# Optimization experiments

Measured on AMD Instinct MI355X. Metric: run time of the kernel, lower is better.

## Reference

```python
import jax, jax.numpy as jnp
import numpy as np
from jax import lax

KS = 3
N = KS * KS  # 9 sampling points per output pixel
EPS = 1e-5
DN = ('NCHW', 'OIHW', 'NCHW')


def _deform_conv(x, w_off, b_off, w_conv):
    """Pure-PyTorch-style DeformConv2d (padding=0, stride=1, no modulation)."""
    b, c, H, W = x.shape
    dt = x.dtype
    # offset conv: 3x3, padding=1 -> (b, 2N, h, w) with h=H, w=W
    offset = lax.conv_general_dilated(x, w_off, (1, 1), ((1, 1), (1, 1)), dimension_numbers=DN)
    offset = offset + b_off[None, :, None, None]
    h, w = offset.shape[2], offset.shape[3]
    # p_n: kernel-relative offsets in {-1,0,1}^2
    r = jnp.arange(-(KS - 1) // 2, (KS - 1) // 2 + 1, dtype=dt)
    pnx, pny = jnp.meshgrid(r, r, indexing='ij')
    p_n = jnp.concatenate([pnx.ravel(), pny.ravel()]).reshape(1, 2 * N, 1, 1)
    # p_0: base grid starting at 1 (faithful to reference impl)
    p0x, p0y = jnp.meshgrid(jnp.arange(1, h + 1, dtype=dt), jnp.arange(1, w + 1, dtype=dt), indexing='ij')
    p_0 = jnp.concatenate([jnp.broadcast_to(p0x, (N, h, w)), jnp.broadcast_to(p0y, (N, h, w))], 0)[None]
    p = p_0 + p_n + offset                      # (b, 2N, h, w)
    p = jnp.transpose(p, (0, 2, 3, 1))          # (b, h, w, 2N)
    # integer corners use detached p (q = floor(p.detach()))
    q = jnp.floor(lax.stop_gradient(p))
    q_lt_x = jnp.clip(q[..., :N], 0, H - 1).astype(jnp.int32)
    q_lt_y = jnp.clip(q[..., N:], 0, W - 1).astype(jnp.int32)
    q_rb_x = jnp.clip(q[..., :N] + 1, 0, H - 1).astype(jnp.int32)
    q_rb_y = jnp.clip(q[..., N:] + 1, 0, W - 1).astype(jnp.int32)
    px = jnp.clip(p[..., :N], 0, H - 1)
    py = jnp.clip(p[..., N:], 0, W - 1)
    flt_x = q_lt_x.astype(dt); flt_y = q_lt_y.astype(dt)
    frb_x = q_rb_x.astype(dt); frb_y = q_rb_y.astype(dt)
    g_lt = (1 + (flt_x - px)) * (1 + (flt_y - py))
    g_rb = (1 - (frb_x - px)) * (1 - (frb_y - py))
    g_lb = (1 + (flt_x - px)) * (1 - (frb_y - py))
    g_rt = (1 - (frb_x - px)) * (1 + (flt_y - py))
    xf = x.reshape(b, c, H * W)

    def gath(qx, qy):
        idx = qx * W + qy                       # (b, h, w, N)
        return jax.vmap(lambda xi, ii: xi[:, ii])(xf, idx)  # (b, c, h, w, N)

    x_off = (g_lt[:, None] * gath(q_lt_x, q_lt_y) +
             g_rb[:, None] * gath(q_rb_x, q_rb_y) +
             g_lb[:, None] * gath(q_lt_x, q_rb_y) +
             g_rt[:, None] * gath(q_rb_x, q_lt_y))  # (b, c, h, w, N)
    # (b, c, h, w, ks1, ks2) -> (b, c, h*ks, w*ks), matching _reshape_x_offset
    x_off = x_off.reshape(b, c, h, w, KS, KS).transpose(0, 1, 2, 4, 3, 5).reshape(b, c, h * KS, w * KS)
    # final conv: kernel ks, stride ks, no bias
    return lax.conv_general_dilated(x_off, w_conv, (KS, KS), ((0, 0), (0, 0)), dimension_numbers=DN)


def _bn_relu(y, gamma, beta):
    mu = y.mean(axis=(0, 2, 3), keepdims=True)
    var = y.var(axis=(0, 2, 3), keepdims=True)  # biased, as PyTorch BN forward
    yn = (y - mu) * lax.rsqrt(var + EPS)
    return jax.nn.relu(yn * gamma[None, :, None, None] + beta[None, :, None, None])


def setup_inputs() -> dict:
    key = jax.random.key(0)
    ks = jax.random.split(key, 8)
    B, IN_CH, OUT_CH, H, W = 2, 64, 64, 224, 224
    x = jax.random.normal(ks[0], (B, IN_CH, H, W), dtype=jnp.float32)
    # offset-predicting convs: small weights => modest, realistic offsets
    w_off1 = jax.random.normal(ks[1], (2 * N, IN_CH, 3, 3), dtype=jnp.float32) * 0.01
    b_off1 = jnp.zeros((2 * N,), dtype=jnp.float32)
    w_conv1 = jax.random.normal(ks[2], (OUT_CH, IN_CH, KS, KS), dtype=jnp.float32) * 0.05
    gamma1 = jnp.ones((OUT_CH,), dtype=jnp.float32)
    beta1 = jnp.zeros((OUT_CH,), dtype=jnp.float32)
    w_off2 = jax.random.normal(ks[3], (2 * N, OUT_CH, 3, 3), dtype=jnp.float32) * 0.01
    b_off2 = jnp.zeros((2 * N,), dtype=jnp.float32)
    w_conv2 = jax.random.normal(ks[4], (OUT_CH, OUT_CH, KS, KS), dtype=jnp.float32) * 0.05
    gamma2 = jnp.ones((OUT_CH,), dtype=jnp.float32)
    beta2 = jnp.zeros((OUT_CH,), dtype=jnp.float32)
    return {"x": x, "w_off1": w_off1, "b_off1": b_off1, "w_conv1": w_conv1,
            "gamma1": gamma1, "beta1": beta1, "w_off2": w_off2, "b_off2": b_off2,
            "w_conv2": w_conv2, "gamma2": gamma2, "beta2": beta2}


def reference(x, w_off1, b_off1, w_conv1, gamma1, beta1,
              w_off2, b_off2, w_conv2, gamma2, beta2):
    y = _deform_conv(x, w_off1, b_off1, w_conv1)
    y = _bn_relu(y, gamma1, beta1)
    y = _deform_conv(y, w_off2, b_off2, w_conv2)
    y = _bn_relu(y, gamma2, beta2)
    return y
```

## Files before the change

kernel.cpp:

```cpp
#include <hip/hip_runtime.h>

#define H 224
#define W 224
#define HW (H*W)
#define BATCH 2
#define CIN 64
#define COUT 64
#define NOFF 18
#define K576 576
#define KCHUNK 288
#define AROW 296
#define OFFS 20
#define NBLK (BATCH*HW/32)
#define NB8  (NBLK/8)
#define TROW 56
#define TCOL 28
#define XROW 68

typedef __attribute__((ext_vector_type(8))) short bf16x8;
typedef __attribute__((ext_vector_type(4))) short s16x4;
typedef __attribute__((ext_vector_type(4))) float f32x4;

__device__ inline short f2bf(float f) {
    unsigned u = __float_as_uint(f);
    u += 0x7FFF + ((u >> 16) & 1);
    return (short)(u >> 16);
}
__device__ inline float bf2f(short h) {
    return __uint_as_float(((unsigned)(unsigned short)h) << 16);
}
__device__ inline void split_bf(float x, short& hi, short& lo) {
    hi = f2bf(x);
    lo = f2bf(x - bf2f(hi));
}
__device__ inline void split_bf4(float a, float b, float c, float d,
                                 s16x4& h4, s16x4& l4) {
    short h0, l0, h1, l1, h2, l2, h3, l3;
    split_bf(a, h0, l0); split_bf(b, h1, l1);
    split_bf(c, h2, l2); split_bf(d, h3, l3);
    h4 = (s16x4){h0, h1, h2, h3};
    l4 = (s16x4){l0, l1, l2, l3};
}
__device__ inline int swizzle_blk(int raw) {
    return (raw & 7) * NB8 + (raw >> 3);
}
__device__ __forceinline__ float f4get(float4 v, int k) {
    switch (k & 3) { case 0: return v.x; case 1: return v.y; case 2: return v.z; default: return v.w; }
}

__global__ __launch_bounds__(256) void k_prepw(const float* __restrict__ wconv,
                                               const float* __restrict__ woff,
                                               short* __restrict__ Wtdh,
                                               short* __restrict__ Wtdl,
                                               short* __restrict__ Wtoh,
                                               short* __restrict__ Wtol) {
    int t = blockIdx.x * 256 + threadIdx.x;
    if (t < COUT * K576) {
        int e = t & 7, lane = (t >> 3) & 63, rest = t >> 9;
        int nt = rest & 3, kt9 = rest >> 2;
        int kt = kt9 % 9, chunk = kt9 / 9;
        int n = nt * 16 + (lane & 15);
        int c = chunk * 32 + (lane >> 4) * 8 + e;
        short h, l; split_bf(wconv[n * K576 + c * 9 + kt], h, l);
        Wtdh[t] = h; Wtdl[t] = l;
    }
    int t2 = t - COUT * K576;
    if (t2 >= 0 && t2 < 32 * K576) {
        int e = t2 & 7, lane = (t2 >> 3) & 63, rest = t2 >> 9;
        int ntb = rest & 1, kt9 = rest >> 1;
        int kt = kt9 % 9, chunk = kt9 / 9;
        int n = ntb * 16 + (lane & 15);
        int c = chunk * 32 + (lane >> 4) * 8 + e;
        float v = (n < NOFF) ? woff[n * K576 + c * 9 + kt] : 0.0f;
        short h, l; split_bf(v, h, l);
        Wtoh[t2] = h; Wtol[t2] = l;
    }
}

__global__ __launch_bounds__(256) void k_transpose(const float* __restrict__ x,
                                                   float* __restrict__ xT) {
    __shared__ float Lt[64][65];
    int blk = blockIdx.x, t = threadIdx.x;
    int px0 = blk * 64;
    int b   = px0 / HW;
    int ij0 = px0 - b * HW;
    int lane = t & 63, g = t >> 6;
#pragma unroll
    for (int r = 0; r < 16; ++r) {
        int c = r * 4 + g;
        Lt[c][lane] = x[(b * CIN + c) * HW + ij0 + lane];
    }
    __syncthreads();
#pragma unroll
    for (int r = 0; r < 16; ++r) {
        int px = r * 4 + g;
        xT[((size_t)(b * HW + ij0 + px)) * 64 + lane] = Lt[lane][px];
    }
}

template <bool OUT_NHWC>
__global__ __launch_bounds__(256, 2) void k_fused(const float* __restrict__ xT,
                                                  const short* __restrict__ Wtoh,
                                                  const short* __restrict__ Wtol,
                                                  const float* __restrict__ boff,
                                                  const short* __restrict__ Wtdh,
                                                  const short* __restrict__ Wtdl,
                                                  float* __restrict__ out,
                                                  float* __restrict__ part) {
    __shared__ __align__(16) char smem[2 * 32 * AROW * 2 + 96 * XROW * 4 + 32 * OFFS * 4];
    short* Ah   = (short*)smem;
    short* Al   = Ah + 32 * AROW;
    float* Xs   = (float*)(smem + 2 * 32 * AROW * 2);
    float* offL = (float*)(smem + 2 * 32 * AROW * 2 + 96 * XROW * 4);

    const int t    = threadIdx.x;
    const int lane = t & 63;
    const int wave = t >> 6;
    const int vb   = swizzle_blk(blockIdx.x);
    const int b    = vb / (TROW * TCOL);
    const int rem  = vb - b * (TROW * TCOL);
    const int i0   = (rem / TCOL) * 4;
    const int j0   = (rem % TCOL) * 8;
    const int spx  = t & 31;
    const int cg   = t >> 5;
    const int pr   = spx >> 3, pc = spx & 7;
    const int i    = i0 + pr, j = j0 + pc;
    const int l15  = lane & 15;
    const int quad = lane >> 4;
    const int mtb  = wave >> 1;
    const int ntb  = wave & 1;

    const float* xb = xT + (size_t)(b * HW) * 64;

#pragma unroll
    for (int k = 0; k < 6; ++k) {
        int idx = k * 256 + t;
        int slot = idx >> 4, e = idx & 15;
        int sr = slot / 12, sc = slot - sr * 12;
        int rr = min(max(i0 - 1 + sr, 0), H - 1);
        int cc = min(max(j0 - 1 + sc, 0), W - 1);
        float4 v = *(const float4*)(xb + (size_t)(rr * W + cc) * 64 + e * 4);
        *(float4*)&Xs[slot * XROW + e * 4] = v;
    }
    __syncthreads();

    int okm = 0;
#pragma unroll
    for (int n = 0; n < 9; ++n) {
        int ii = i + n / 3 - 1, jj = j + n % 3 - 1;
        okm |= (int)((ii >= 0) & (ii < H) & (jj >= 0) & (jj < W)) << n;
    }

    f32x4 aoc = (f32x4){0.f, 0.f, 0.f, 0.f};

    for (int chunk = 0; chunk < 2; ++chunk) {
        short* wrh = &Ah[spx * AROW + cg * 4];
        short* wrl = &Al[spx * AROW + cg * 4];
#pragma unroll
        for (int n = 0; n < 9; ++n) {
            int slot = (pr + n / 3) * 12 + (pc + n % 3);
            float4 v = make_float4(0.f, 0.f, 0.f, 0.f);
            if ((okm >> n) & 1) v = *(float4*)&Xs[slot * XROW + chunk * 32 + cg * 4];
            s16x4 h4, l4;
            split_bf4(v.x, v.y, v.z, v.w, h4, l4);
            *(s16x4*)(wrh + n * 32) = h4;
            *(s16x4*)(wrl + n * 32) = l4;
        }
        __syncthreads();
        const short* aph = &Ah[(mtb * 16 + l15) * AROW + quad * 8];
        const short* apl = &Al[(mtb * 16 + l15) * AROW + quad * 8];
#pragma unroll
        for (int kt = 0; kt < 9; ++kt) {
            bf16x8 afh = *(const bf16x8*)(aph + kt * 32);
            bf16x8 afl = *(const bf16x8*)(apl + kt * 32);
            int fb = ((chunk * 9 + kt) * 2 + ntb) * 512 + lane * 8;
            bf16x8 bfh = *(const bf16x8*)(Wtoh + fb);
            bf16x8 bfl = *(const bf16x8*)(Wtol + fb);
            aoc = __builtin_amdgcn_mfma_f32_16x16x32_bf16(afh, bfh, aoc, 0, 0, 0);
            aoc = __builtin_amdgcn_mfma_f32_16x16x32_bf16(afl, bfh, aoc, 0, 0, 0);
            aoc = __builtin_amdgcn_mfma_f32_16x16x32_bf16(afh, bfl, aoc, 0, 0, 0);
        }
        __syncthreads();
    }
    {
        int n = ntb * 16 + l15;
        if (n < OFFS) {
            float bi = (n < NOFF) ? boff[n] : 0.0f;
            int pxr = mtb * 16 + quad * 4;
#pragma unroll
            for (int r = 0; r < 4; ++r)
                offL[(pxr + r) * OFFS + n] = aoc[r] + bi;
        }
    }
    __syncthreads();

    const float4 ofA = *(float4*)&offL[spx * OFFS + 0];
    const float4 ofB = *(float4*)&offL[spx * OFFS + 4];
    const float4 ofC = *(float4*)&offL[spx * OFFS + 8];
    const float4 ofD = *(float4*)&offL[spx * OFFS + 12];
    const float4 ofE = *(float4*)&offL[spx * OFFS + 16];
#define OFFSEL(idx) ((idx) < 4 ? f4get(ofA, (idx)) : (idx) < 8 ? f4get(ofB, (idx)-4) : \
                     (idx) < 12 ? f4get(ofC, (idx)-8) : (idx) < 16 ? f4get(ofD, (idx)-12) : f4get(ofE, (idx)-16))

    f32x4 acc[2];
    acc[0] = (f32x4){0.f, 0.f, 0.f, 0.f};
    acc[1] = (f32x4){0.f, 0.f, 0.f, 0.f};
    const int ntb0 = (wave & 1) * 2;

    for (int chunk = 0; chunk < 2; ++chunk) {
        const int ch = chunk * 32 + cg * 4;
        short* wrh = &Ah[spx * AROW + cg * 4];
        short* wrl = &Al[spx * AROW + cg * 4];
#pragma unroll
        for (int n = 0; n < 9; ++n) {
            float px_f = (float)(i + n / 3) + OFFSEL(n);
            float py_f = (float)(j + n % 3) + OFFSEL(9 + n);
            float qx = floorf(px_f), qy = floorf(py_f);
            int ltx = min(max((int)qx, 0), H - 1);
            int lty = min(max((int)qy, 0), W - 1);
            int rbx = min(max((int)qx + 1, 0), H - 1);
            int rby = min(max((int)qy + 1, 0), W - 1);
            float px = fminf(fmaxf(px_f, 0.0f), (float)(H - 1));
            float py = fminf(fmaxf(py_f, 0.0f), (float)(W - 1));
            float alt = 1.0f + ((float)ltx - px);
            float arb = 1.0f - ((float)rbx - px);
            float blt = 1.0f + ((float)lty - py);
            float brb = 1.0f - ((float)rby - py);
            float g0 = alt * blt, g1 = arb * brb, g2 = alt * brb, g3 = arb * blt;
            int slr = ltx - (i0 - 1), srr = rbx - (i0 - 1);
            int slc = lty - (j0 - 1), src = rby - (j0 - 1);
            float4 v0, v1, v2, v3;
            if (((unsigned)slr < 8u) & ((unsigned)srr < 8u) &
                ((unsigned)slc < 12u) & ((unsigned)src < 12u)) {
                v0 = *(float4*)&Xs[(slr * 12 + slc) * XROW + ch];
                v1 = *(float4*)&Xs[(srr * 12 + src) * XROW + ch];
                v2 = *(float4*)&Xs[(slr * 12 + src) * XROW + ch];
                v3 = *(float4*)&Xs[(srr * 12 + slc) * XROW + ch];
            } else {
                v0 = *(const float4*)(xb + (size_t)(ltx * W + lty) * 64 + ch);
                v1 = *(const float4*)(xb + (size_t)(rbx * W + rby) * 64 + ch);
                v2 = *(const float4*)(xb + (size_t)(ltx * W + rby) * 64 + ch);
                v3 = *(const float4*)(xb + (size_t)(rbx * W + lty) * 64 + ch);
            }
            float s0 = g0 * v0.x + g1 * v1.x + g2 * v2.x + g3 * v3.x;
            float s1 = g0 * v0.y + g1 * v1.y + g2 * v2.y + g3 * v3.y;
            float s2 = g0 * v0.z + g1 * v1.z + g2 * v2.z + g3 * v3.z;
            float s3 = g0 * v0.w + g1 * v1.w + g2 * v2.w + g3 * v3.w;
            s16x4 h4, l4;
            split_bf4(s0, s1, s2, s3, h4, l4);
            *(s16x4*)(wrh + n * 32) = h4;
            *(s16x4*)(wrl + n * 32) = l4;
        }
        __syncthreads();
        const short* aph = &Ah[(mtb * 16 + l15) * AROW + quad * 8];
        const short* apl = &Al[(mtb * 16 + l15) * AROW + quad * 8];
#pragma unroll
        for (int kt = 0; kt < 9; ++kt) {
            bf16x8 afh = *(const bf16x8*)(aph + kt * 32);
            bf16x8 afl = *(const bf16x8*)(apl + kt * 32);
#pragma unroll
            for (int nt = 0; nt < 2; ++nt) {
                int fb = ((chunk * 9 + kt) * 4 + ntb0 + nt) * 512 + lane * 8;
                bf16x8 bfh = *(const bf16x8*)(Wtdh + fb);
                bf16x8 bfl = *(const bf16x8*)(Wtdl + fb);
                acc[nt] = __builtin_amdgcn_mfma_f32_16x16x32_bf16(afh, bfh, acc[nt], 0, 0, 0);
                acc[nt] = __builtin_amdgcn_mfma_f32_16x16x32_bf16(afl, bfh, acc[nt], 0, 0, 0);
                acc[nt] = __builtin_amdgcn_mfma_f32_16x16x32_bf16(afh, bfl, acc[nt], 0, 0, 0);
            }
        }
        __syncthreads();
    }
#undef OFFSEL

    float* Ld = (float*)smem;
    if (OUT_NHWC) {
        int pxr = mtb * 16 + quad * 4;
#pragma unroll
        for (int nt = 0; nt < 2; ++nt) {
            int c = (ntb0 + nt) * 16 + l15;
#pragma unroll
            for (int r = 0; r < 4; ++r)
                Ld[(pxr + r) * 72 + c] = acc[nt][r];
        }
        __syncthreads();
#pragma unroll
        for (int r = 0; r < 2; ++r) {
            int px = (t >> 4) + r * 16, c4 = t & 15;
            float4 v = *(float4*)&Ld[px * 72 + c4 * 4];
            int pij = (i0 + (px >> 3)) * W + j0 + (px & 7);
            *(float4*)(out + (size_t)(b * HW + pij) * 64 + c4 * 4) = v;
        }
    } else {
        int pxr = mtb * 16 + quad * 4;
#pragma unroll
        for (int nt = 0; nt < 2; ++nt) {
            int c = (ntb0 + nt) * 16 + l15;
#pragma unroll
            for (int r = 0; r < 4; ++r)
                Ld[c * 36 + pxr + r] = acc[nt][r];
        }
        __syncthreads();
#pragma unroll
        for (int cc = 0; cc < 2; ++cc) {
            int c = cc * 32 + (t >> 3), p4 = t & 7;
            float4 v = *(float4*)&Ld[c * 36 + p4 * 4];
            int px = p4 * 4;
            int pij = (i0 + (px >> 3)) * W + j0 + (px & 7);
            *(float4*)(out + (size_t)(b * COUT + c) * HW + pij) = v;
        }
    }
    {
        float* Sr = Xs;
        int c = t & 63, g = t >> 6;
        float s = 0.f, q = 0.f;
#pragma unroll
        for (int k = 0; k < 8; ++k) {
            int px = g * 8 + k;
            float v = OUT_NHWC ? Ld[px * 72 + c] : Ld[c * 36 + px];
            s += v; q += v * v;
        }
        Sr[g * 64 + c]       = s;
        Sr[256 + g * 64 + c] = q;
        __syncthreads();
        if (t < 64) {
            float ts = Sr[t] + Sr[64 + t] + Sr[128 + t] + Sr[192 + t];
            float tq = Sr[256 + t] + Sr[320 + t] + Sr[384 + t] + Sr[448 + t];
            part[(size_t)blockIdx.x * 128 + t]      = ts;
            part[(size_t)blockIdx.x * 128 + 64 + t] = tq;
        }
    }
}

__global__ __launch_bounds__(256) void k_stats2(const float* __restrict__ part,
                                                const float* __restrict__ gamma,
                                                const float* __restrict__ beta,
                                                float* __restrict__ ss) {
    int c = blockIdx.x, t = threadIdx.x;
    float s = 0.f, q = 0.f;
    for (int k = t; k < NBLK; k += 256) {
        s += part[(size_t)k * 128 + c];
        q += part[(size_t)k * 128 + 64 + c];
    }
#pragma unroll
    for (int d = 32; d > 0; d >>= 1) {
        s += __shfl_down(s, d, 64);
        q += __shfl_down(q, d, 64);
    }
    __shared__ float red[8];
    int wv = t >> 6;
    if ((t & 63) == 0) { red[wv] = s; red[4 + wv] = q; }
    __syncthreads();
    if (t == 0) {
        float ts = red[0] + red[1] + red[2] + red[3];
        float tq = red[4] + red[5] + red[6] + red[7];
        const float inv_m = 1.0f / (float)(BATCH * HW);
        float mu    = ts * inv_m;
        float var   = tq * inv_m - mu * mu;
        float scale = rsqrtf(var + 1e-5f) * gamma[c];
        ss[c]      = scale;
        ss[64 + c] = beta[c] - mu * scale;
    }
}

__global__ __launch_bounds__(256) void k_bnrelu_nhwc(const float* __restrict__ y,
                                                     const float* __restrict__ ss,
                                                     float* __restrict__ out) {
    size_t idx = ((size_t)blockIdx.x * 256 + threadIdx.x) * 4;
    int c4 = (int)(idx & 63);
    float4 sc = *(const float4*)(ss + c4);
    float4 sh = *(const float4*)(ss + 64 + c4);
    float4 v  = *(const float4*)(y + idx);
    float4 r;
    r.x = fmaxf(fmaf(v.x, sc.x, sh.x), 0.f);
    r.y = fmaxf(fmaf(v.y, sc.y, sh.y), 0.f);
    r.z = fmaxf(fmaf(v.z, sc.z, sh.z), 0.f);
    r.w = fmaxf(fmaf(v.w, sc.w, sh.w), 0.f);
    *(float4*)(out + idx) = r;
}

__global__ __launch_bounds__(256) void k_bnrelu_nchw(float* __restrict__ y,
                                                     const float* __restrict__ ss) {
    int c = (blockIdx.x / 49) % COUT;
    float scale = ss[c], shift = ss[64 + c];
    size_t idx = ((size_t)blockIdx.x * 1024) + threadIdx.x * 4;
    float4 v = *(const float4*)(y + idx);
    float4 r;
    r.x = fmaxf(fmaf(v.x, scale, shift), 0.f);
    r.y = fmaxf(fmaf(v.y, scale, shift), 0.f);
    r.z = fmaxf(fmaf(v.z, scale, shift), 0.f);
    r.w = fmaxf(fmaf(v.w, scale, shift), 0.f);
    *(float4*)(y + idx) = r;
}

extern "C" void kernel_launch(void* const* d_in, const int* in_sizes, int n_in,
                              void* d_out, int out_size, void* d_ws, size_t ws_size,
                              hipStream_t stream) {
    const float* x       = (const float*)d_in[0];
    const float* w_off1  = (const float*)d_in[1];
    const float* b_off1  = (const float*)d_in[2];
    const float* w_conv1 = (const float*)d_in[3];
    const float* gamma1  = (const float*)d_in[4];
    const float* beta1   = (const float*)d_in[5];
    const float* w_off2  = (const float*)d_in[6];
    const float* b_off2  = (const float*)d_in[7];
    const float* w_conv2 = (const float*)d_in[8];
    const float* gamma2  = (const float*)d_in[9];
    const float* beta2   = (const float*)d_in[10];
    float* out = (float*)d_out;

    char*  wsb  = (char*)d_ws;
    short* Wtdh = (short*)wsb;
    short* Wtdl = (short*)(wsb + 73728);
    short* Wtoh = (short*)(wsb + 147456);
    short* Wtol = (short*)(wsb + 184320);
    float* part = (float*)(wsb + 221184);
    float* ss   = (float*)(wsb + 1826816);
    float* bufB = (float*)(wsb + 1827328);

    const int tp_blocks = (BATCH * HW) / 64;
    const int bn_blocks = (BATCH * COUT * HW) / 1024;

    k_prepw       <<<216, 256, 0, stream>>>(w_conv1, w_off1, Wtdh, Wtdl, Wtoh, Wtol);
    k_transpose   <<<tp_blocks, 256, 0, stream>>>(x, bufB);
    k_fused<true> <<<NBLK, 256, 0, stream>>>(bufB, Wtoh, Wtol, b_off1, Wtdh, Wtdl, out, part);
    k_stats2      <<<64, 256, 0, stream>>>(part, gamma1, beta1, ss);
    k_bnrelu_nhwc <<<bn_blocks, 256, 0, stream>>>(out, ss, bufB);

    k_prepw       <<<216, 256, 0, stream>>>(w_conv2, w_off2, Wtdh, Wtdl, Wtoh, Wtol);
    k_fused<false><<<NBLK, 256, 0, stream>>>(bufB, Wtoh, Wtol, b_off2, Wtdh, Wtdl, out, part);
    k_stats2      <<<64, 256, 0, stream>>>(part, gamma2, beta2, ss);
    k_bnrelu_nchw <<<bn_blocks, 256, 0, stream>>>(out, ss);
}
```

Before: 342.4 us.

## Use 8x8 pixel tiles and build MFMA A-fragments in registers

Each block now covers an 8x8 pixel tile (64 pixels) instead of 4x8, and each wave owns 16 pixels across all output channels. The A operands for both the offset conv and the deformable conv are formed directly in registers from the staged input and the bilinear samples, instead of being written as bf16 hi/lo to shared memory and read back. This removes the A-staging shared buffers and most barriers, shrinking LDS so occupancy can rise (launch bounds raised to 4 blocks per CU). In exchange each wave issues more MFMAs and weight loads per block, and the larger halo tile changes the fallback rate to global gathers.

```diff
diff --git a/kernel.cpp b/kernel.cpp
--- a/kernel.cpp
+++ b/kernel.cpp
@@ -8,14 +8,14 @@
 #define COUT 64
 #define NOFF 18
 #define K576 576
-#define KCHUNK 288
-#define AROW 296
 #define OFFS 20
-#define NBLK (BATCH*HW/32)
+#define NBLK (BATCH*HW/64)
 #define NB8  (NBLK/8)
-#define TROW 56
-#define TCOL 28
+#define TC8  28
 #define XROW 68
+#define PRW 10
+#define PCW 10
+#define LDROW 72
 
 typedef __attribute__((ext_vector_type(8))) short bf16x8;
 typedef __attribute__((ext_vector_type(4))) short s16x4;
@@ -40,6 +40,15 @@
     split_bf(c, h2, l2); split_bf(d, h3, l3);
     h4 = (s16x4){h0, h1, h2, h3};
     l4 = (s16x4){l0, l1, l2, l3};
+}
+__device__ inline void split_bf8(float a0, float a1, float a2, float a3,
+                                 float a4, float a5, float a6, float a7,
+                                 bf16x8& hi, bf16x8& lo) {
+    s16x4 h0, l0, h1, l1;
+    split_bf4(a0, a1, a2, a3, h0, l0);
+    split_bf4(a4, a5, a6, a7, h1, l1);
+    hi = __builtin_shufflevector(h0, h1, 0, 1, 2, 3, 4, 5, 6, 7);
+    lo = __builtin_shufflevector(l0, l1, 0, 1, 2, 3, 4, 5, 6, 7);
 }
 __device__ inline int swizzle_blk(int raw) {
     return (raw & 7) * NB8 + (raw >> 3);
@@ -99,7 +108,7 @@
 }
 
 template <bool OUT_NHWC>
-__global__ __launch_bounds__(256, 2) void k_fused(const float* __restrict__ xT,
+__global__ __launch_bounds__(256, 4) void k_fused(const float* __restrict__ xT,
                                                   const short* __restrict__ Wtoh,
                                                   const short* __restrict__ Wtol,
                                                   const float* __restrict__ boff,
@@ -107,160 +116,147 @@
                                                   const short* __restrict__ Wtdl,
                                                   float* __restrict__ out,
                                                   float* __restrict__ part) {
-    __shared__ __align__(16) char smem[2 * 32 * AROW * 2 + 96 * XROW * 4 + 32 * OFFS * 4];
-    short* Ah   = (short*)smem;
-    short* Al   = Ah + 32 * AROW;
-    float* Xs   = (float*)(smem + 2 * 32 * AROW * 2);
-    float* offL = (float*)(smem + 2 * 32 * AROW * 2 + 96 * XROW * 4);
+    __shared__ __align__(16) char smem[PRW * PCW * XROW * 4 + 64 * OFFS * 4];
+    float* Xs   = (float*)smem;
+    float* offL = (float*)(smem + PRW * PCW * XROW * 4);
 
     const int t    = threadIdx.x;
     const int lane = t & 63;
-    const int wave = t >> 6;
-    const int vb   = swizzle_blk(blockIdx.x);
-    const int b    = vb / (TROW * TCOL);
-    const int rem  = vb - b * (TROW * TCOL);
-    const int i0   = (rem / TCOL) * 4;
-    const int j0   = (rem % TCOL) * 8;
-    const int spx  = t & 31;
-    const int cg   = t >> 5;
-    const int pr   = spx >> 3, pc = spx & 7;
-    const int i    = i0 + pr, j = j0 + pc;
+    const int wv   = t >> 6;
     const int l15  = lane & 15;
     const int quad = lane >> 4;
-    const int mtb  = wave >> 1;
-    const int ntb  = wave & 1;
+    const int vb   = swizzle_blk(blockIdx.x);
+    const int b    = vb / (TC8 * TC8);
+    const int rem  = vb - b * (TC8 * TC8);
+    const int i0   = (rem / TC8) * 8;
+    const int j0   = (rem % TC8) * 8;
+    const int lp   = wv * 16 + l15;
+    const int i    = i0 + (lp >> 3);
+    const int j    = j0 + (lp & 7);
 
     const float* xb = xT + (size_t)(b * HW) * 64;
 
 #pragma unroll
-    for (int k = 0; k < 6; ++k) {
+    for (int k = 0; k < 7; ++k) {
         int idx = k * 256 + t;
-        int slot = idx >> 4, e = idx & 15;
-        int sr = slot / 12, sc = slot - sr * 12;
-        int rr = min(max(i0 - 1 + sr, 0), H - 1);
-        int cc = min(max(j0 - 1 + sc, 0), W - 1);
-        float4 v = *(const float4*)(xb + (size_t)(rr * W + cc) * 64 + e * 4);
-        *(float4*)&Xs[slot * XROW + e * 4] = v;
+        if (idx < PRW * PCW * 16) {
+            int slot = idx >> 4, e = idx & 15;
+            int sr = slot / PCW, sc = slot - sr * PCW;
+            int rr = min(max(i0 - 1 + sr, 0), H - 1);
+            int cc = min(max(j0 - 1 + sc, 0), W - 1);
+            *(float4*)&Xs[slot * XROW + e * 4] =
+                *(const float4*)(xb + (size_t)(rr * W + cc) * 64 + e * 4);
+        }
     }
     __syncthreads();
 
-    int okm = 0;
-#pragma unroll
-    for (int n = 0; n < 9; ++n) {
-        int ii = i + n / 3 - 1, jj = j + n % 3 - 1;
-        okm |= (int)((ii >= 0) & (ii < H) & (jj >= 0) & (jj < W)) << n;
-    }
-
-    f32x4 aoc = (f32x4){0.f, 0.f, 0.f, 0.f};
-
-    for (int chunk = 0; chunk < 2; ++chunk) {
-        short* wrh = &Ah[spx * AROW + cg * 4];
-        short* wrl = &Al[spx * AROW + cg * 4];
-#pragma unroll
-        for (int n = 0; n < 9; ++n) {
-            int slot = (pr + n / 3) * 12 + (pc + n % 3);
-            float4 v = make_float4(0.f, 0.f, 0.f, 0.f);
-            if ((okm >> n) & 1) v = *(float4*)&Xs[slot * XROW + chunk * 32 + cg * 4];
-            s16x4 h4, l4;
-            split_bf4(v.x, v.y, v.z, v.w, h4, l4);
-            *(s16x4*)(wrh + n * 32) = h4;
-            *(s16x4*)(wrl + n * 32) = l4;
-        }
-        __syncthreads();
-        const short* aph = &Ah[(mtb * 16 + l15) * AROW + quad * 8];
-        const short* apl = &Al[(mtb * 16 + l15) * AROW + quad * 8];
-#pragma unroll
-        for (int kt = 0; kt < 9; ++kt) {
-            bf16x8 afh = *(const bf16x8*)(aph + kt * 32);
-            bf16x8 afl = *(const bf16x8*)(apl + kt * 32);
-            int fb = ((chunk * 9 + kt) * 2 + ntb) * 512 + lane * 8;
-            bf16x8 bfh = *(const bf16x8*)(Wtoh + fb);
-            bf16x8 bfl = *(const bf16x8*)(Wtol + fb);
-            aoc = __builtin_amdgcn_mfma_f32_16x16x32_bf16(afh, bfh, aoc, 0, 0, 0);
-            aoc = __builtin_amdgcn_mfma_f32_16x16x32_bf16(afl, bfh, aoc, 0, 0, 0);
-            aoc = __builtin_amdgcn_mfma_f32_16x16x32_bf16(afh, bfl, aoc, 0, 0, 0);
-        }
-        __syncthreads();
+    f32x4 aoc0 = (f32x4){0.f, 0.f, 0.f, 0.f};
+    f32x4 aoc1 = (f32x4){0.f, 0.f, 0.f, 0.f};
+#pragma unroll
+    for (int kt = 0; kt < 9; ++kt) {
+        const int di = kt / 3, dj = kt % 3;
+        const int ii = i + di - 1, jj = j + dj - 1;
+        const bool ok = (ii >= 0) && (ii < H) && (jj >= 0) && (jj < W);
+        const float* xp = &Xs[(((lp >> 3) + di) * PCW + (lp & 7) + dj) * XROW + quad * 8];
+#pragma unroll
+        for (int chunk = 0; chunk < 2; ++chunk) {
+            float4 va = make_float4(0.f, 0.f, 0.f, 0.f), vb4 = va;
+            if (ok) {
+                va  = *(const float4*)(xp + chunk * 32);
+                vb4 = *(const float4*)(xp + chunk * 32 + 4);
+            }
+            bf16x8 afh, afl;
+            split_bf8(va.x, va.y, va.z, va.w, vb4.x, vb4.y, vb4.z, vb4.w, afh, afl);
+            const int fb = (chunk * 9 + kt) * 2 * 512 + lane * 8;
+            bf16x8 bh0 = *(const bf16x8*)(Wtoh + fb);
+            bf16x8 bl0 = *(const bf16x8*)(Wtol + fb);
+            aoc0 = __builtin_amdgcn_mfma_f32_16x16x32_bf16(afh, bh0, aoc0, 0, 0, 0);
+            aoc0 = __builtin_amdgcn_mfma_f32_16x16x32_bf16(afl, bh0, aoc0, 0, 0, 0);
+            aoc0 = __builtin_amdgcn_mfma_f32_16x16x32_bf16(afh, bl0, aoc0, 0, 0, 0);
+            bf16x8 bh1 = *(const bf16x8*)(Wtoh + fb + 512);
+            bf16x8 bl1 = *(const bf16x8*)(Wtol + fb + 512);
+            aoc1 = __builtin_amdgcn_mfma_f32_16x16x32_bf16(afh, bh1, aoc1, 0, 0, 0);
+            aoc1 = __builtin_amdgcn_mfma_f32_16x16x32_bf16(afl, bh1, aoc1, 0, 0, 0);
+            aoc1 = __builtin_amdgcn_mfma_f32_16x16x32_bf16(afh, bl1, aoc1, 0, 0, 0);
+        }
     }
     {
-        int n = ntb * 16 + l15;
-        if (n < OFFS) {
-            float bi = (n < NOFF) ? boff[n] : 0.0f;
-            int pxr = mtb * 16 + quad * 4;
+        const int pr0 = wv * 16 + quad * 4;
+        const float bi = boff[l15];
+#pragma unroll
+        for (int r = 0; r < 4; ++r)
+            offL[(pr0 + r) * OFFS + l15] = aoc0[r] + bi;
+        if (l15 < 2) {
+            const float bi2 = boff[16 + l15];
 #pragma unroll
             for (int r = 0; r < 4; ++r)
-                offL[(pxr + r) * OFFS + n] = aoc[r] + bi;
+                offL[(pr0 + r) * OFFS + 16 + l15] = aoc1[r] + bi2;
         }
     }
     __syncthreads();
 
-    const float4 ofA = *(float4*)&offL[spx * OFFS + 0];
-    const float4 ofB = *(float4*)&offL[spx * OFFS + 4];
-    const float4 ofC = *(float4*)&offL[spx * OFFS + 8];
-    const float4 ofD = *(float4*)&offL[spx * OFFS + 12];
-    const float4 ofE = *(float4*)&offL[spx * OFFS + 16];
+    const float* ofp = &offL[(wv * 16 + l15) * OFFS];
+    const float4 ofA = *(const float4*)(ofp + 0);
+    const float4 ofB = *(const float4*)(ofp + 4);
+    const float4 ofC = *(const float4*)(ofp + 8);
+    const float4 ofD = *(const float4*)(ofp + 12);
+    const float4 ofE = *(const float4*)(ofp + 16);
 #define OFFSEL(idx) ((idx) < 4 ? f4get(ofA, (idx)) : (idx) < 8 ? f4get(ofB, (idx)-4) : \
                      (idx) < 12 ? f4get(ofC, (idx)-8) : (idx) < 16 ? f4get(ofD, (idx)-12) : f4get(ofE, (idx)-16))
 
-    f32x4 acc[2];
+    f32x4 acc[4];
     acc[0] = (f32x4){0.f, 0.f, 0.f, 0.f};
-    acc[1] = (f32x4){0.f, 0.f, 0.f, 0.f};
-    const int ntb0 = (wave & 1) * 2;
-
-    for (int chunk = 0; chunk < 2; ++chunk) {
-        const int ch = chunk * 32 + cg * 4;
-        short* wrh = &Ah[spx * AROW + cg * 4];
-        short* wrl = &Al[spx * AROW + cg * 4];
-#pragma unroll
-        for (int n = 0; n < 9; ++n) {
-            float px_f = (float)(i + n / 3) + OFFSEL(n);
-            float py_f = (float)(j + n % 3) + OFFSEL(9 + n);
-            float qx = floorf(px_f), qy = floorf(py_f);
-            int ltx = min(max((int)qx, 0), H - 1);
-            int lty = min(max((int)qy, 0), W - 1);
-            int rbx = min(max((int)qx + 1, 0), H - 1);
-            int rby = min(max((int)qy + 1, 0), W - 1);
-            float px = fminf(fmaxf(px_f, 0.0f), (float)(H - 1));
-            float py = fminf(fmaxf(py_f, 0.0f), (float)(W - 1));
-            float alt = 1.0f + ((float)ltx - px);
-            float arb = 1.0f - ((float)rbx - px);
-            float blt = 1.0f + ((float)lty - py);
-            float brb = 1.0f - ((float)rby - py);
-            float g0 = alt * blt, g1 = arb * brb, g2 = alt * brb, g3 = arb * blt;
-            int slr = ltx - (i0 - 1), srr = rbx - (i0 - 1);
-            int slc = lty - (j0 - 1), src = rby - (j0 - 1);
-            float4 v0, v1, v2, v3;
-            if (((unsigned)slr < 8u) & ((unsigned)srr < 8u) &
-                ((unsigned)slc < 12u) & ((unsigned)src < 12u)) {
-                v0 = *(float4*)&Xs[(slr * 12 + slc) * XROW + ch];
-                v1 = *(float4*)&Xs[(srr * 12 + src) * XROW + ch];
-                v2 = *(float4*)&Xs[(slr * 12 + src) * XROW + ch];
-                v3 = *(float4*)&Xs[(srr * 12 + slc) * XROW + ch];
-            } else {
-                v0 = *(const float4*)(xb + (size_t)(ltx * W + lty) * 64 + ch);
-                v1 = *(const float4*)(xb + (size_t)(rbx * W + rby) * 64 + ch);
-                v2 = *(const float4*)(xb + (size_t)(ltx * W + rby) * 64 + ch);
-                v3 = *(const float4*)(xb + (size_t)(rbx * W + lty) * 64 + ch);
+    acc[1] = acc[0]; acc[2] = acc[0]; acc[3] = acc[0];
+
+#pragma unroll
+    for (int kt = 0; kt < 9; ++kt) {
+        float px_f = (float)(i + kt / 3) + OFFSEL(kt);
+        float py_f = (float)(j + kt % 3) + OFFSEL(9 + kt);
+        float qx = floorf(px_f), qy = floorf(py_f);
+        int ltx = min(max((int)qx, 0), H - 1);
+        int lty = min(max((int)qy, 0), W - 1);
+        int rbx = min(max((int)qx + 1, 0), H - 1);
+        int rby = min(max((int)qy + 1, 0), W - 1);
+        float cpx = fminf(fmaxf(px_f, 0.0f), (float)(H - 1));
+        float cpy = fminf(fmaxf(py_f, 0.0f), (float)(W - 1));
+        float alt = 1.0f + ((float)ltx - cpx);
+        float arb = 1.0f - ((float)rbx - cpx);
+        float blt = 1.0f + ((float)lty - cpy);
+        float brb = 1.0f - ((float)rby - cpy);
+        float g0 = alt * blt, g1 = arb * brb, g2 = alt * brb, g3 = arb * blt;
+        int slr = ltx - (i0 - 1), srr = rbx - (i0 - 1);
+        int slc = lty - (j0 - 1), src = rby - (j0 - 1);
+        const bool inp = ((unsigned)slr < (unsigned)PRW) & ((unsigned)srr < (unsigned)PRW) &
+                         ((unsigned)slc < (unsigned)PCW) & ((unsigned)src < (unsigned)PCW);
+#pragma unroll
+        for (int chunk = 0; chunk < 2; ++chunk) {
+            const int ch = chunk * 32 + quad * 8;
+            float s[8];
+#pragma unroll
+            for (int hf = 0; hf < 2; ++hf) {
+                const int cho = ch + hf * 4;
+                float4 v0, v1, v2, v3;
+                if (inp) {
+                    v0 = *(const float4*)&Xs[(slr * PCW + slc) * XROW + cho];
+                    v1 = *(const float4*)&Xs[(srr * PCW + src) * XROW + cho];
+                    v2 = *(const float4*)&Xs[(slr * PCW + src) * XROW + cho];
+                    v3 = *(const float4*)&Xs[(srr * PCW + slc) * XROW + cho];
+                } else {
+                    v0 = *(const float4*)(xb + (size_t)(ltx * W + lty) * 64 + cho);
+                    v1 = *(const float4*)(xb + (size_t)(rbx * W + rby) * 64 + cho);
+                    v2 = *(const float4*)(xb + (size_t)(ltx * W + rby) * 64 + cho);
+                    v3 = *(const float4*)(xb + (size_t)(rbx * W + lty) * 64 + cho);
+                }
+                s[hf * 4 + 0] = g0 * v0.x + g1 * v1.x + g2 * v2.x + g3 * v3.x;
+                s[hf * 4 + 1] = g0 * v0.y + g1 * v1.y + g2 * v2.y + g3 * v3.y;
+                s[hf * 4 + 2] = g0 * v0.z + g1 * v1.z + g2 * v2.z + g3 * v3.z;
+                s[hf * 4 + 3] = g0 * v0.w + g1 * v1.w + g2 * v2.w + g3 * v3.w;
             }
-            float s0 = g0 * v0.x + g1 * v1.x + g2 * v2.x + g3 * v3.x;
-            float s1 = g0 * v0.y + g1 * v1.y + g2 * v2.y + g3 * v3.y;
-            float s2 = g0 * v0.z + g1 * v1.z + g2 * v2.z + g3 * v3.z;
-            float s3 = g0 * v0.w + g1 * v1.w + g2 * v2.w + g3 * v3.w;
-            s16x4 h4, l4;
-            split_bf4(s0, s1, s2, s3, h4, l4);
-            *(s16x4*)(wrh + n * 32) = h4;
-            *(s16x4*)(wrl + n * 32) = l4;
-        }
-        __syncthreads();
-        const short* aph = &Ah[(mtb * 16 + l15) * AROW + quad * 8];
-        const short* apl = &Al[(mtb * 16 + l15) * AROW + quad * 8];
-#pragma unroll
-        for (int kt = 0; kt < 9; ++kt) {
-            bf16x8 afh = *(const bf16x8*)(aph + kt * 32);
-            bf16x8 afl = *(const bf16x8*)(apl + kt * 32);
-#pragma unroll
-            for (int nt = 0; nt < 2; ++nt) {
-                int fb = ((chunk * 9 + kt) * 4 + ntb0 + nt) * 512 + lane * 8;
+            bf16x8 afh, afl;
+            split_bf8(s[0], s[1], s[2], s[3], s[4], s[5], s[6], s[7], afh, afl);
+#pragma unroll
+            for (int nt = 0; nt < 4; ++nt) {
+                const int fb = ((chunk * 9 + kt) * 4 + nt) * 512 + lane * 8;
                 bf16x8 bfh = *(const bf16x8*)(Wtdh + fb);
                 bf16x8 bfl = *(const bf16x8*)(Wtdl + fb);
                 acc[nt] = __builtin_amdgcn_mfma_f32_16x16x32_bf16(afh, bfh, acc[nt], 0, 0, 0);
@@ -268,56 +264,64 @@
                 acc[nt] = __builtin_amdgcn_mfma_f32_16x16x32_bf16(afh, bfl, acc[nt], 0, 0, 0);
             }
         }
+    }
+#undef OFFSEL
+
+    __syncthreads();
+    float* Ld = Xs;
+    const int pr0 = wv * 16 + quad * 4;
+    if (OUT_NHWC) {
+#pragma unroll
+        for (int nt = 0; nt < 4; ++nt) {
+            int c = nt * 16 + l15;
+#pragma unroll
+            for (int r = 0; r < 4; ++r)
+                Ld[(pr0 + r) * LDROW + c] = acc[nt][r];
+        }
         __syncthreads();
-    }
-#undef OFFSEL
-
-    float* Ld = (float*)smem;
-    if (OUT_NHWC) {
-        int pxr = mtb * 16 + quad * 4;
-#pragma unroll
-        for (int nt = 0; nt < 2; ++nt) {
-            int c = (ntb0 + nt) * 16 + l15;
-#pragma unroll
-            for (int r = 0; r < 4; ++r)
-                Ld[(pxr + r) * 72 + c] = acc[nt][r];
-        }
-        __syncthreads();
-#pragma unroll
-        for (int r = 0; r < 2; ++r) {
-            int px = (t >> 4) + r * 16, c4 = t & 15;
-            float4 v = *(float4*)&Ld[px * 72 + c4 * 4];
+#pragma unroll
+        for (int it = 0; it < 4; ++it) {
+            int idx = it * 256 + t;
+            int px = idx >> 4, c4 = idx & 15;
+            float4 v = *(float4*)&Ld[px * LDROW + c4 * 4];
             int pij = (i0 + (px >> 3)) * W + j0 + (px & 7);
             *(float4*)(out + (size_t)(b * HW + pij) * 64 + c4 * 4) = v;
         }
     } else {
-        int pxr = mtb * 16 + quad * 4;
-#pragma unroll
-        for (int nt = 0; nt < 2; ++nt) {
-            int c = (ntb0 + nt) * 16 + l15;
+#pragma unroll
+        for (int nt = 0; nt < 4; ++nt) {
+            int c = nt * 16 + l15;
 #pragma unroll
             for (int r = 0; r < 4; ++r)
-                Ld[c * 36 + pxr + r] = acc[nt][r];
+                Ld[c * LDROW + pr0 + r] = acc[nt][r];
         }
         __syncthreads();
 #pragma unroll
-        for (int cc = 0; cc < 2; ++cc) {
-            int c = cc * 32 + (t >> 3), p4 = t & 7;
-            float4 v = *(float4*)&Ld[c * 36 + p4 * 4];
-            int px = p4 * 4;
-            int pij = (i0 + (px >> 3)) * W + j0 + (px & 7);
+        for (int it = 0; it < 4; ++it) {
+            int idx = it * 256 + t;
+            int c = idx >> 4, p4 = idx & 15;
+            float4 v = *(float4*)&Ld[c * LDROW + p4 * 4];
+            int pij = (i0 + (p4 >> 1)) * W + j0 + (p4 & 1) * 4;
             *(float4*)(out + (size_t)(b * COUT + c) * HW + pij) = v;
         }
     }
     {
-        float* Sr = Xs;
+        float* Sr = offL;
         int c = t & 63, g = t >> 6;
         float s = 0.f, q = 0.f;
-#pragma unroll
-        for (int k = 0; k < 8; ++k) {
-            int px = g * 8 + k;
-            float v = OUT_NHWC ? Ld[px * 72 + c] : Ld[c * 36 + px];
-            s += v; q += v * v;
+        if (OUT_NHWC) {
+#pragma unroll
+            for (int k = 0; k < 16; ++k) {
+                float v = Ld[(g * 16 + k) * LDROW + c];
+                s += v; q += v * v;
+            }
+        } else {
+#pragma unroll
+            for (int k4 = 0; k4 < 4; ++k4) {
+                float4 v = *(const float4*)&Ld[c * LDROW + g * 16 + k4 * 4];
+                s += v.x + v.y + v.z + v.w;
+                q += v.x * v.x + v.y * v.y + v.z * v.z + v.w * v.w;
+            }
         }
         Sr[g * 64 + c]       = s;
         Sr[256 + g * 64 + c] = q;
```

New measurement: 305.8 us. 10.7% less time.
